# Optimization experiments

Measured on AMD Instinct MI355X. Metric: run time of the kernel, lower is better.

The kernel has to match this reference:

```python
import jax, jax.numpy as jnp
import numpy as np

B, N, H, W, NHOR = 4096, 128, 128, 64, 3

def setup_inputs() -> dict:
    key = jax.random.key(0)
    ks = jax.random.split(key, 11)
    s = 1.0 / np.sqrt(H)
    return {
        "embeddings": jax.random.normal(ks[0], (B, H), jnp.float32),
        "sensor_embeddings": jax.random.normal(ks[1], (B, N, H), jnp.float32),
        "sensor_logits": jax.random.normal(ks[2], (B, N), jnp.float32),
        "fc1_w": jax.random.normal(ks[3], (H, H), jnp.float32) * s,
        "fc1_b": jax.random.normal(ks[4], (H,), jnp.float32) * s,
        "fc2_w": jax.random.normal(ks[5], (NHOR * N, H), jnp.float32) * s,
        "fc2_b": jax.random.normal(ks[6], (NHOR * N,), jnp.float32) * s,
        "rw1": jax.random.normal(ks[7], (N, H, H), jnp.float32) * s,
        "rb1": jax.random.normal(ks[8], (N, H), jnp.float32) * s,
        "rw2": jax.random.normal(ks[9], (N, H, W), jnp.float32) * s,
        "rb2": jax.random.normal(ks[10], (N, W), jnp.float32) * s,
    }

def reference(embeddings, sensor_embeddings, sensor_logits,
              fc1_w, fc1_b, fc2_w, fc2_b, rw1, rb1, rw2, rb2):
    # Forecasting head: Linear -> ReLU -> (Dropout: identity in eval) -> Linear
    h = jax.nn.relu(embeddings @ fc1_w.T + fc1_b)              # (B, H)
    forecast = (h @ fc2_w.T + fc2_b).reshape(-1, NHOR, N)      # (B, NHOR, N)
    # Reconstruction heads: per-node MLPs batched as stacked GEMMs
    hn = jax.nn.relu(jnp.einsum('bnh,nhk->bnk', sensor_embeddings, rw1) + rb1)  # (B, N, H)
    recon = jnp.einsum('bnk,nkw->bnw', hn, rw2) + rb2          # (B, N, W)
    reconstruction = jnp.transpose(recon, (0, 2, 1))           # (B, W, N), matches torch.stack(dim=2)
    return (sensor_logits, forecast, reconstruction)
```

## Files before the change

### kernel.cpp

```cpp
#include <hip/hip_runtime.h>
#include <hip/hip_bf16.h>
#include <stdint.h>

typedef __attribute__((ext_vector_type(8))) short bf16x8;
typedef __attribute__((ext_vector_type(4))) float f32x4;

#define DEVI static __device__ __forceinline__

static constexpr int B_SZ = 4096, N_SZ = 128, H_SZ = 128, W_SZ = 64;

static constexpr size_t OFF_W1 = 0;
static constexpr size_t OFF_W2 = OFF_W1 + 4194304;
static constexpr size_t OFF_F1 = OFF_W2 + 2097152;
static constexpr size_t OFF_F2 = OFF_F1 + 32768;
static constexpr size_t OFF_H  = OFF_F2 + 98304;

DEVI unsigned short f2bf(float f) {
  union { __hip_bfloat16 b; unsigned short u; } cv;
  cv.b = __float2bfloat16(f);
  return cv.u;
}
DEVI float bf2f(unsigned short u) {
  union { unsigned int i; float f; } cv;
  cv.i = ((unsigned int)u) << 16;
  return cv.f;
}

DEVI void bar_lds() {
  __builtin_amdgcn_sched_barrier(0);
  asm volatile("s_waitcnt lgkmcnt(0)" ::: "memory");
  __builtin_amdgcn_s_barrier();
  __builtin_amdgcn_sched_barrier(0);
}

DEVI bf16x8 frag_ld(const unsigned char* base, int row, int kslot) {
  return *reinterpret_cast<const bf16x8*>(base + row * 256 + (((kslot ^ (row & 7)) << 4)));
}
DEVI bf16x8 gfrag_ld(const unsigned char* base, int row, int kslot) {
  return *reinterpret_cast<const bf16x8*>(base + row * 256 + (kslot << 4));
}

DEVI void stage_f32_tile(const float* src, int row_stride, unsigned char* dst, int tid, int nrows) {
  for (int t = tid; t < nrows * 16; t += 256) {
    int row = t >> 4, s = t & 15;
    const float* p = src + (size_t)row * row_stride + s * 8;
    union { unsigned short u[8]; uint4 v; } pk;
#pragma unroll
    for (int j = 0; j < 8; ++j) pk.u[j] = f2bf(p[j]);
    *reinterpret_cast<uint4*>(dst + row * 256 + ((s ^ (row & 7)) << 4)) = pk.v;
  }
}

__global__ __launch_bounds__(256) void prep_kernel(const float* __restrict__ rw1,
                                                   const float* __restrict__ rw2,
                                                   const float* __restrict__ fc1w,
                                                   const float* __restrict__ fc2w,
                                                   unsigned char* __restrict__ ws) {
  const int T_W1 = 128 * 128 * 16;
  const int T_W2 = 128 * 64 * 16;
  const int T_F1 = 128 * 16;
  const int T_F2 = 384 * 16;
  int id = blockIdx.x * 256 + threadIdx.x;
  if (id < T_W1) {
    int c = id & 127, rest = id >> 7;
    int s = rest & 15, n = rest >> 4;
    const float* src = rw1 + (size_t)n * 16384 + (size_t)(s * 8) * 128 + c;
    union { unsigned short u[8]; uint4 v; } pk;
#pragma unroll
    for (int j = 0; j < 8; ++j) pk.u[j] = f2bf(src[(size_t)j * 128]);
    size_t dst = OFF_W1 + ((size_t)n * 128 + c) * 256 + (size_t)(s << 4);
    *reinterpret_cast<uint4*>(ws + dst) = pk.v;
    return;
  }
  id -= T_W1;
  if (id < T_W2) {
    int w = id & 63, rest = id >> 6;
    int s = rest & 15, n = rest >> 4;
    const float* src = rw2 + (size_t)n * 8192 + (size_t)(s * 8) * 64 + w;
    union { unsigned short u[8]; uint4 v; } pk;
#pragma unroll
    for (int j = 0; j < 8; ++j) pk.u[j] = f2bf(src[(size_t)j * 64]);
    size_t dst = OFF_W2 + ((size_t)n * 64 + w) * 256 + (size_t)(s << 4);
    *reinterpret_cast<uint4*>(ws + dst) = pk.v;
    return;
  }
  id -= T_W2;
  if (id < T_F1) {
    int s = id & 15, o = id >> 4;
    const float* src = fc1w + (size_t)o * 128 + s * 8;
    union { unsigned short u[8]; uint4 v; } pk;
#pragma unroll
    for (int j = 0; j < 8; ++j) pk.u[j] = f2bf(src[j]);
    *reinterpret_cast<uint4*>(ws + OFF_F1 + (size_t)o * 256 + ((s ^ (o & 7)) << 4)) = pk.v;
    return;
  }
  id -= T_F1;
  if (id < T_F2) {
    int s = id & 15, o = id >> 4;
    const float* src = fc2w + (size_t)o * 128 + s * 8;
    union { unsigned short u[8]; uint4 v; } pk;
#pragma unroll
    for (int j = 0; j < 8; ++j) pk.u[j] = f2bf(src[j]);
    *reinterpret_cast<uint4*>(ws + OFF_F2 + (size_t)o * 256 + ((s ^ (o & 7)) << 4)) = pk.v;
  }
}

__global__ __launch_bounds__(256, 2) void recon_kernel(const float* __restrict__ se,
                                                       const float* __restrict__ rb1,
                                                       const float* __restrict__ rb2,
                                                       const unsigned char* __restrict__ ws,
                                                       float* __restrict__ out3) {
  __shared__ unsigned char sSE[2][16384];
  __shared__ unsigned char sHN[16384];

  const int tid = threadIdx.x;
  const int n = blockIdx.x;
  const int btg = blockIdx.y;
  const int b0 = btg * 512;

  const int wave = tid >> 6, lane = tid & 63;
  const int wm = wave >> 1, wq = wave & 1;
  const int lr = lane & 15, lk = lane >> 4;

  const unsigned char* w1b = ws + OFF_W1 + (size_t)n * 32768;
  const unsigned char* w2b = ws + OFF_W2 + (size_t)n * 16384;
  bf16x8 w1f[4][4], w2f[2][4];
#pragma unroll
  for (int m = 0; m < 4; ++m)
#pragma unroll
    for (int kk = 0; kk < 4; ++kk)
      w1f[m][kk] = gfrag_ld(w1b, wm * 64 + m * 16 + lr, kk * 4 + lk);
#pragma unroll
  for (int m = 0; m < 2; ++m)
#pragma unroll
    for (int kk = 0; kk < 4; ++kk)
      w2f[m][kk] = gfrag_ld(w2b, wm * 32 + m * 16 + lr, kk * 4 + lk);

  float bias1[4][4], bias2[2][4];
#pragma unroll
  for (int m = 0; m < 4; ++m)
#pragma unroll
    for (int j = 0; j < 4; ++j) bias1[m][j] = rb1[(size_t)n * 128 + wm * 64 + m * 16 + lk * 4 + j];
#pragma unroll
  for (int m = 0; m < 2; ++m)
#pragma unroll
    for (int j = 0; j < 4; ++j) bias2[m][j] = rb2[(size_t)n * 64 + wm * 32 + m * 16 + lk * 4 + j];

  stage_f32_tile(se + ((size_t)b0 * 128 + n) * 128, 128 * 128, sSE[0], tid, 64);
  unsigned short* outus = reinterpret_cast<unsigned short*>(out3);

  float4 fra[4], frb[4];
  {
    const float* sb = se + ((size_t)(b0 + 64) * 128 + n) * 128;
#pragma unroll
    for (int k = 0; k < 4; ++k) {
      int c = tid + k * 256;
      int row = c >> 4, s = c & 15;
      const float* p = sb + (size_t)row * 16384 + s * 8;
      fra[k] = *reinterpret_cast<const float4*>(p);
      frb[k] = *reinterpret_cast<const float4*>(p + 4);
    }
  }
  __syncthreads();

#pragma unroll 1
  for (int t = 0; t < 8; ++t) {
    unsigned char* bufc = sSE[t & 1];
    unsigned char* bufn = sSE[(t + 1) & 1];

    f32x4 acc[4][2] = {};
#pragma unroll
    for (int kk = 0; kk < 4; ++kk) {
      const int slot = kk * 4 + lk;
      bf16x8 bv[2];
#pragma unroll
      for (int q = 0; q < 2; ++q) bv[q] = frag_ld(bufc, wq * 32 + q * 16 + lr, slot);
#pragma unroll
      for (int m = 0; m < 4; ++m)
#pragma unroll
        for (int q = 0; q < 2; ++q)
          acc[m][q] = __builtin_amdgcn_mfma_f32_16x16x32_bf16(w1f[m][kk], bv[q], acc[m][q], 0, 0, 0);
    }
    bar_lds();

#pragma unroll
    for (int m = 0; m < 4; ++m) {
      const int k0 = wm * 64 + m * 16 + lk * 4;
      const int s16 = k0 >> 3, half = (k0 >> 2) & 1;
#pragma unroll
      for (int q = 0; q < 2; ++q) {
        const int b = wq * 32 + q * 16 + lr;
        union { unsigned short u[4]; uint2 v; } pk;
#pragma unroll
        for (int j = 0; j < 4; ++j) {
          float v = acc[m][q][j] + bias1[m][j];
          v = v > 0.f ? v : 0.f;
          pk.u[j] = f2bf(v);
        }
        *reinterpret_cast<uint2*>(sHN + b * 256 + ((s16 ^ (b & 7)) << 4) + half * 8) = pk.v;
      }
    }

    if (t < 7) {
#pragma unroll
      for (int k = 0; k < 4; ++k) {
        int c = tid + k * 256;
        int row = c >> 4, s = c & 15;
        union { unsigned short u[8]; uint4 v; } pk;
#pragma unroll
        for (int j = 0; j < 4; ++j) pk.u[j] = f2bf(fra[k][j]);
#pragma unroll
        for (int j = 0; j < 4; ++j) pk.u[4 + j] = f2bf(frb[k][j]);
        *reinterpret_cast<uint4*>(bufn + row * 256 + ((s ^ (row & 7)) << 4)) = pk.v;
      }
    }
    if (t < 6) {
      const float* sb = se + ((size_t)(b0 + (t + 2) * 64) * 128 + n) * 128;
#pragma unroll
      for (int k = 0; k < 4; ++k) {
        int c = tid + k * 256;
        int row = c >> 4, s = c & 15;
        const float* p = sb + (size_t)row * 16384 + s * 8;
        fra[k] = *reinterpret_cast<const float4*>(p);
        frb[k] = *reinterpret_cast<const float4*>(p + 4);
      }
    }
    bar_lds();

    f32x4 acc2[2][2] = {};
#pragma unroll
    for (int kk = 0; kk < 4; ++kk) {
      const int slot = kk * 4 + lk;
      bf16x8 bv[2];
#pragma unroll
      for (int q = 0; q < 2; ++q) bv[q] = frag_ld(sHN, wq * 32 + q * 16 + lr, slot);
#pragma unroll
      for (int m = 0; m < 2; ++m)
#pragma unroll
        for (int q = 0; q < 2; ++q)
          acc2[m][q] = __builtin_amdgcn_mfma_f32_16x16x32_bf16(w2f[m][kk], bv[q], acc2[m][q], 0, 0, 0);
    }

    const int bt0 = b0 + t * 64;
#pragma unroll
    for (int m = 0; m < 2; ++m) {
      const int w0 = wm * 32 + m * 16 + lk * 4;
#pragma unroll
      for (int q = 0; q < 2; ++q) {
        const int b = bt0 + wq * 32 + q * 16 + lr;
        union { unsigned short u[4]; uint2 v; } pk;
#pragma unroll
        for (int j = 0; j < 4; ++j) pk.u[j] = f2bf(acc2[m][q][j] + bias2[m][j]);
        *reinterpret_cast<uint2*>(outus + (size_t)b * 16384 + 8192 + n * 64 + w0) = pk.v;
      }
    }
  }
}

__global__ __launch_bounds__(256) void transpose_kernel(float* __restrict__ out3) {
  const int b = blockIdx.x, wave = threadIdx.x >> 6, lane = threadIdx.x & 63;
  const unsigned short* t = reinterpret_cast<const unsigned short*>(out3) + (size_t)b * 16384 + 8192;
  float* dst = out3 + (size_t)b * 8192;
  uint4 r[2][2];
#pragma unroll
  for (int half = 0; half < 2; ++half) {
    const int g = half * 4 + wave;
    r[half][0] = *reinterpret_cast<const uint4*>(t + lane * 64 + g * 8);
    r[half][1] = *reinterpret_cast<const uint4*>(t + (size_t)(lane + 64) * 64 + g * 8);
  }
  __syncthreads();
#pragma unroll
  for (int half = 0; half < 2; ++half) {
    const int g = half * 4 + wave;
    union { uint4 v; unsigned short u[8]; } p0, p1;
    p0.v = r[half][0];
    p1.v = r[half][1];
#pragma unroll
    for (int j = 0; j < 8; ++j) {
      dst[(g * 8 + j) * 128 + lane] = bf2f(p0.u[j]);
      dst[(g * 8 + j) * 128 + lane + 64] = bf2f(p1.u[j]);
    }
  }
}

__global__ __launch_bounds__(256) void f1_kernel(const float* __restrict__ emb,
                                                 const float* __restrict__ fc1b,
                                                 const unsigned char* __restrict__ ws,
                                                 unsigned char* __restrict__ hsw) {
  __shared__ unsigned char sA[32768];
  __shared__ unsigned char sB[32768];
  const int tid = threadIdx.x;
  const int bt = blockIdx.x;
  const int b0 = bt * 128;
  {
    const uint4* wp = reinterpret_cast<const uint4*>(ws + OFF_F1);
    uint4* d = reinterpret_cast<uint4*>(sB);
    for (int c = tid; c < 2048; c += 256) d[c] = wp[c];
  }
  stage_f32_tile(emb + (size_t)b0 * 128, 128, sA, tid, 128);
  __syncthreads();

  const int wave = tid >> 6, lane = tid & 63;
  const int wm = wave >> 1, wn = wave & 1;
  const int lr = lane & 15, lk = lane >> 4;

  f32x4 acc[4][4] = {};
#pragma unroll
  for (int kk = 0; kk < 4; ++kk) {
    bf16x8 af[4], bfv[4];
#pragma unroll
    for (int m = 0; m < 4; ++m) af[m] = frag_ld(sA, wm * 64 + m * 16 + lr, kk * 4 + lk);
#pragma unroll
    for (int q = 0; q < 4; ++q) bfv[q] = frag_ld(sB, wn * 64 + q * 16 + lr, kk * 4 + lk);
#pragma unroll
    for (int m = 0; m < 4; ++m)
#pragma unroll
      for (int q = 0; q < 4; ++q)
        acc[m][q] = __builtin_amdgcn_mfma_f32_16x16x32_bf16(af[m], bfv[q], acc[m][q], 0, 0, 0);
  }

  unsigned char* tile = hsw + (size_t)bt * 32768;
#pragma unroll
  for (int q = 0; q < 4; ++q) {
    int c = wn * 64 + q * 16 + lr;
    float bias = fc1b[c];
#pragma unroll
    for (int m = 0; m < 4; ++m) {
#pragma unroll
      for (int j = 0; j < 4; ++j) {
        int r = wm * 64 + m * 16 + lk * 4 + j;
        float v = acc[m][q][j] + bias;
        v = v > 0.f ? v : 0.f;
        *reinterpret_cast<unsigned short*>(tile + r * 256 + ((c * 2) ^ ((r & 7) << 4))) = f2bf(v);
      }
    }
  }
}

__global__ __launch_bounds__(256) void f2_kernel(const unsigned char* __restrict__ hsw,
                                                 const unsigned char* __restrict__ f2s,
                                                 const float* __restrict__ fc2b,
                                                 float* __restrict__ out2) {
  __shared__ unsigned char sA[32768];
  __shared__ unsigned char sB[32768];
  const int tid = threadIdx.x;
  const int bt = blockIdx.x;
  const int ch = blockIdx.y;
  const int b0 = bt * 128;
  {
    const uint4* ap = reinterpret_cast<const uint4*>(hsw + (size_t)bt * 32768);
    uint4* da = reinterpret_cast<uint4*>(sA);
    for (int c = tid; c < 2048; c += 256) da[c] = ap[c];
    const uint4* bp = reinterpret_cast<const uint4*>(f2s + (size_t)ch * 32768);
    uint4* db = reinterpret_cast<uint4*>(sB);
    for (int c = tid; c < 2048; c += 256) db[c] = bp[c];
  }
  __syncthreads();

  const int wave = tid >> 6, lane = tid & 63;
  const int wm = wave >> 1, wn = wave & 1;
  const int lr = lane & 15, lk = lane >> 4;

  f32x4 acc[4][4] = {};
#pragma unroll
  for (int kk = 0; kk < 4; ++kk) {
    bf16x8 af[4], bfv[4];
#pragma unroll
    for (int m = 0; m < 4; ++m) af[m] = frag_ld(sA, wm * 64 + m * 16 + lr, kk * 4 + lk);
#pragma unroll
    for (int q = 0; q < 4; ++q) bfv[q] = frag_ld(sB, wn * 64 + q * 16 + lr, kk * 4 + lk);
#pragma unroll
    for (int m = 0; m < 4; ++m)
#pragma unroll
      for (int q = 0; q < 4; ++q)
        acc[m][q] = __builtin_amdgcn_mfma_f32_16x16x32_bf16(af[m], bfv[q], acc[m][q], 0, 0, 0);
  }

#pragma unroll
  for (int q = 0; q < 4; ++q) {
    int o = ch * 128 + wn * 64 + q * 16 + lr;
    float bias = fc2b[o];
#pragma unroll
    for (int m = 0; m < 4; ++m) {
#pragma unroll
      for (int j = 0; j < 4; ++j) {
        int r = wm * 64 + m * 16 + lk * 4 + j;
        out2[(size_t)(b0 + r) * 384 + o] = acc[m][q][j] + bias;
      }
    }
  }
}

extern "C" void kernel_launch(void* const* d_in, const int* in_sizes, int n_in,
                              void* d_out, int out_size, void* d_ws, size_t ws_size,
                              hipStream_t stream) {
  const float* emb  = (const float*)d_in[0];
  const float* se   = (const float*)d_in[1];
  const float* slog = (const float*)d_in[2];
  const float* fc1w = (const float*)d_in[3];
  const float* fc1b = (const float*)d_in[4];
  const float* fc2w = (const float*)d_in[5];
  const float* fc2b = (const float*)d_in[6];
  const float* rw1  = (const float*)d_in[7];
  const float* rb1  = (const float*)d_in[8];
  const float* rw2  = (const float*)d_in[9];
  const float* rb2  = (const float*)d_in[10];
  float* out = (float*)d_out;
  unsigned char* ws = (unsigned char*)d_ws;

  hipMemcpyAsync(out, slog, (size_t)B_SZ * N_SZ * sizeof(float),
                 hipMemcpyDeviceToDevice, stream);

  prep_kernel<<<1568, 256, 0, stream>>>(rw1, rw2, fc1w, fc2w, ws);

  f1_kernel<<<32, 256, 0, stream>>>(emb, fc1b, ws, ws + OFF_H);
  f2_kernel<<<dim3(32, 3), 256, 0, stream>>>(ws + OFF_H, ws + OFF_F2, fc2b,
                                             out + (size_t)B_SZ * N_SZ);

  float* out3 = out + (size_t)B_SZ * N_SZ + (size_t)B_SZ * 384;
  recon_kernel<<<dim3(128, 8), 256, 0, stream>>>(se, rb1, rb2, ws, out3);
  transpose_kernel<<<4096, 256, 0, stream>>>(out3);
}
```

Measured before the change: 138.9 us.

## Stage sensor embeddings via async global-to-LDS loads and fold logits copy into prep

Replaces the register-staged fp32 loads, conversion and LDS stores of the sensor-embedding tiles with async global_load_lds transfers that write raw fp32 into a larger, swizzled double buffer. Conversion to bf16 now happens at fragment-load time, and explicit vmcnt waits pace the pipeline. This aims to free registers and VALU from the staging path and overlap loads better. It also replaces the separate memcpy of sensor_logits with extra threads in prep_kernel to save a launch. The cost is doubled LDS use (64KB for the two buffers plus sHN), which may lower occupancy, and more conversion work inside the MFMA loop.

```diff
diff --git a/kernel.cpp b/kernel.cpp
--- a/kernel.cpp
+++ b/kernel.cpp
@@ -15,6 +15,9 @@
 static constexpr size_t OFF_F2 = OFF_F1 + 32768;
 static constexpr size_t OFF_H  = OFF_F2 + 98304;
 
+typedef const __attribute__((address_space(1))) void gvoid;
+typedef __attribute__((address_space(3))) void lvoid;
+
 DEVI unsigned short f2bf(float f) {
   union { __hip_bfloat16 b; unsigned short u; } cv;
   cv.b = __float2bfloat16(f);
@@ -51,15 +54,32 @@
   }
 }
 
+DEVI void stage_async(const float* se, int brow0, int n, unsigned char* dstbase,
+                      int wave, int lane) {
+  const int rr = lane >> 5;
+  const int g  = lane & 31;
+#pragma unroll
+  for (int c = 0; c < 8; ++c) {
+    const int rl = wave * 16 + c * 2 + rr;
+    const int gsrc = g ^ ((rl & 7) << 1);
+    const float* gp = se + ((size_t)(brow0 + rl) * 128 + n) * 128 + gsrc * 4;
+    unsigned char* lp = dstbase + (wave * 16 + c * 2) * 512;
+    __builtin_amdgcn_global_load_lds((gvoid*)gp, (lvoid*)lp, 16, 0, 0);
+  }
+}
+
 __global__ __launch_bounds__(256) void prep_kernel(const float* __restrict__ rw1,
                                                    const float* __restrict__ rw2,
                                                    const float* __restrict__ fc1w,
                                                    const float* __restrict__ fc2w,
+                                                   const float* __restrict__ slog,
+                                                   float* __restrict__ out,
                                                    unsigned char* __restrict__ ws) {
   const int T_W1 = 128 * 128 * 16;
   const int T_W2 = 128 * 64 * 16;
   const int T_F1 = 128 * 16;
   const int T_F2 = 384 * 16;
+  const int T_LG = 131072;
   int id = blockIdx.x * 256 + threadIdx.x;
   if (id < T_W1) {
     int c = id & 127, rest = id >> 7;
@@ -102,6 +122,11 @@
 #pragma unroll
     for (int j = 0; j < 8; ++j) pk.u[j] = f2bf(src[j]);
     *reinterpret_cast<uint4*>(ws + OFF_F2 + (size_t)o * 256 + ((s ^ (o & 7)) << 4)) = pk.v;
+    return;
+  }
+  id -= T_F2;
+  if (id < T_LG) {
+    reinterpret_cast<uint4*>(out)[id] = reinterpret_cast<const uint4*>(slog)[id];
   }
 }
 
@@ -110,7 +135,7 @@
                                                        const float* __restrict__ rb2,
                                                        const unsigned char* __restrict__ ws,
                                                        float* __restrict__ out3) {
-  __shared__ unsigned char sSE[2][16384];
+  __shared__ unsigned char sSE[2][32768];
   __shared__ unsigned char sHN[16384];
 
   const int tid = threadIdx.x;
@@ -146,27 +171,21 @@
 #pragma unroll
     for (int j = 0; j < 4; ++j) bias2[m][j] = rb2[(size_t)n * 64 + wm * 32 + m * 16 + lk * 4 + j];
 
-  stage_f32_tile(se + ((size_t)b0 * 128 + n) * 128, 128 * 128, sSE[0], tid, 64);
   unsigned short* outus = reinterpret_cast<unsigned short*>(out3);
 
-  float4 fra[4], frb[4];
-  {
-    const float* sb = se + ((size_t)(b0 + 64) * 128 + n) * 128;
-#pragma unroll
-    for (int k = 0; k < 4; ++k) {
-      int c = tid + k * 256;
-      int row = c >> 4, s = c & 15;
-      const float* p = sb + (size_t)row * 16384 + s * 8;
-      fra[k] = *reinterpret_cast<const float4*>(p);
-      frb[k] = *reinterpret_cast<const float4*>(p + 4);
-    }
-  }
-  __syncthreads();
+  stage_async(se, b0, n, sSE[0], wave, lane);
+  stage_async(se, b0 + 64, n, sSE[1], wave, lane);
 
 #pragma unroll 1
   for (int t = 0; t < 8; ++t) {
     unsigned char* bufc = sSE[t & 1];
-    unsigned char* bufn = sSE[(t + 1) & 1];
+
+    __builtin_amdgcn_sched_barrier(0);
+    if (t == 0 || t == 7) asm volatile("s_waitcnt vmcnt(8)" ::: "memory");
+    else if (t == 1)      asm volatile("s_waitcnt vmcnt(12)" ::: "memory");
+    else                  asm volatile("s_waitcnt vmcnt(16)" ::: "memory");
+    __builtin_amdgcn_s_barrier();
+    __builtin_amdgcn_sched_barrier(0);
 
     f32x4 acc[4][2] = {};
 #pragma unroll
@@ -174,7 +193,16 @@
       const int slot = kk * 4 + lk;
       bf16x8 bv[2];
 #pragma unroll
-      for (int q = 0; q < 2; ++q) bv[q] = frag_ld(bufc, wq * 32 + q * 16 + lr, slot);
+      for (int q = 0; q < 2; ++q) {
+        const int b = wq * 32 + q * 16 + lr;
+        const unsigned char* base = bufc + b * 512 + (((2 * slot) ^ ((b & 7) << 1)) << 4);
+        float4 lo = *reinterpret_cast<const float4*>(base);
+        float4 hi = *reinterpret_cast<const float4*>(base + 16);
+        union { unsigned short u[8]; bf16x8 v; } pk;
+        pk.u[0] = f2bf(lo.x); pk.u[1] = f2bf(lo.y); pk.u[2] = f2bf(lo.z); pk.u[3] = f2bf(lo.w);
+        pk.u[4] = f2bf(hi.x); pk.u[5] = f2bf(hi.y); pk.u[6] = f2bf(hi.z); pk.u[7] = f2bf(hi.w);
+        bv[q] = pk.v;
+      }
 #pragma unroll
       for (int m = 0; m < 4; ++m)
 #pragma unroll
@@ -182,6 +210,8 @@
           acc[m][q] = __builtin_amdgcn_mfma_f32_16x16x32_bf16(w1f[m][kk], bv[q], acc[m][q], 0, 0, 0);
     }
     bar_lds();
+
+    if (t < 6) stage_async(se, b0 + (t + 2) * 64, n, bufc, wave, lane);
 
 #pragma unroll
     for (int m = 0; m < 4; ++m) {
@@ -198,31 +228,6 @@
           pk.u[j] = f2bf(v);
         }
         *reinterpret_cast<uint2*>(sHN + b * 256 + ((s16 ^ (b & 7)) << 4) + half * 8) = pk.v;
-      }
-    }
-
-    if (t < 7) {
-#pragma unroll
-      for (int k = 0; k < 4; ++k) {
-        int c = tid + k * 256;
-        int row = c >> 4, s = c & 15;
-        union { unsigned short u[8]; uint4 v; } pk;
-#pragma unroll
-        for (int j = 0; j < 4; ++j) pk.u[j] = f2bf(fra[k][j]);
-#pragma unroll
-        for (int j = 0; j < 4; ++j) pk.u[4 + j] = f2bf(frb[k][j]);
-        *reinterpret_cast<uint4*>(bufn + row * 256 + ((s ^ (row & 7)) << 4)) = pk.v;
-      }
-    }
-    if (t < 6) {
-      const float* sb = se + ((size_t)(b0 + (t + 2) * 64) * 128 + n) * 128;
-#pragma unroll
-      for (int k = 0; k < 4; ++k) {
-        int c = tid + k * 256;
-        int row = c >> 4, s = c & 15;
-        const float* p = sb + (size_t)row * 16384 + s * 8;
-        fra[k] = *reinterpret_cast<const float4*>(p);
-        frb[k] = *reinterpret_cast<const float4*>(p + 4);
       }
     }
     bar_lds();
@@ -408,10 +413,7 @@
   float* out = (float*)d_out;
   unsigned char* ws = (unsigned char*)d_ws;
 
-  hipMemcpyAsync(out, slog, (size_t)B_SZ * N_SZ * sizeof(float),
-                 hipMemcpyDeviceToDevice, stream);
-
-  prep_kernel<<<1568, 256, 0, stream>>>(rw1, rw2, fc1w, fc2w, ws);
+  prep_kernel<<<2080, 256, 0, stream>>>(rw1, rw2, fc1w, fc2w, slog, out, ws);
 
   f1_kernel<<<32, 256, 0, stream>>>(emb, fc1b, ws, ws + OFF_H);
   f2_kernel<<<dim3(32, 3), 256, 0, stream>>>(ws + OFF_H, ws + OFF_F2, fc2b,
```

Result: slower. 147.7 us (+6.4%).

## Merge prep, f1, memcpy into one launch and co-schedule f2 with recon

Applied to the files above, without the earlier changes.

Cuts the launch count from five kernels plus a memcpy down to three. The weight-prep kernel now also copies the sensor logits and runs the fc1 GEMM in extra blocks that convert fc1 weights on the fly. The f2 GEMM runs as extra blocks of the recon kernel and reads its A operand directly from global memory rather than from LDS. Recon now takes its biases from shared memory and reloads its W2 fragments every iteration to lower register pressure, at the cost of more repeated global or L2 reads.

```diff
diff --git a/kernel.cpp b/kernel.cpp
--- a/kernel.cpp
+++ b/kernel.cpp
@@ -51,102 +51,192 @@
   }
 }
 
-__global__ __launch_bounds__(256) void prep_kernel(const float* __restrict__ rw1,
-                                                   const float* __restrict__ rw2,
-                                                   const float* __restrict__ fc1w,
-                                                   const float* __restrict__ fc2w,
-                                                   unsigned char* __restrict__ ws) {
-  const int T_W1 = 128 * 128 * 16;
-  const int T_W2 = 128 * 64 * 16;
-  const int T_F1 = 128 * 16;
-  const int T_F2 = 384 * 16;
-  int id = blockIdx.x * 256 + threadIdx.x;
-  if (id < T_W1) {
-    int c = id & 127, rest = id >> 7;
-    int s = rest & 15, n = rest >> 4;
-    const float* src = rw1 + (size_t)n * 16384 + (size_t)(s * 8) * 128 + c;
-    union { unsigned short u[8]; uint4 v; } pk;
-#pragma unroll
-    for (int j = 0; j < 8; ++j) pk.u[j] = f2bf(src[(size_t)j * 128]);
-    size_t dst = OFF_W1 + ((size_t)n * 128 + c) * 256 + (size_t)(s << 4);
-    *reinterpret_cast<uint4*>(ws + dst) = pk.v;
+__global__ __launch_bounds__(256) void prep_f1_kernel(const float* __restrict__ rw1,
+                                                      const float* __restrict__ rw2,
+                                                      const float* __restrict__ fc2w,
+                                                      const float* __restrict__ slog,
+                                                      const float* __restrict__ emb,
+                                                      const float* __restrict__ fc1w,
+                                                      const float* __restrict__ fc1b,
+                                                      float* __restrict__ out,
+                                                      unsigned char* __restrict__ ws) {
+  __shared__ unsigned char sA[16384];
+  __shared__ unsigned char sB[32768];
+
+  const int bid = blockIdx.x;
+  const int tid = threadIdx.x;
+  if (bid < 2072) {
+    const int T_W1 = 128 * 128 * 16;
+    const int T_W2 = 128 * 64 * 16;
+    const int T_F2 = 384 * 16;
+    int id = bid * 256 + tid;
+    if (id < T_W1) {
+      int c = id & 127, rest = id >> 7;
+      int s = rest & 15, n = rest >> 4;
+      const float* src = rw1 + (size_t)n * 16384 + (size_t)(s * 8) * 128 + c;
+      union { unsigned short u[8]; uint4 v; } pk;
+#pragma unroll
+      for (int j = 0; j < 8; ++j) pk.u[j] = f2bf(src[(size_t)j * 128]);
+      size_t dst = OFF_W1 + ((size_t)n * 128 + c) * 256 + (size_t)(s << 4);
+      *reinterpret_cast<uint4*>(ws + dst) = pk.v;
+      return;
+    }
+    id -= T_W1;
+    if (id < T_W2) {
+      int w = id & 63, rest = id >> 6;
+      int s = rest & 15, n = rest >> 4;
+      const float* src = rw2 + (size_t)n * 8192 + (size_t)(s * 8) * 64 + w;
+      union { unsigned short u[8]; uint4 v; } pk;
+#pragma unroll
+      for (int j = 0; j < 8; ++j) pk.u[j] = f2bf(src[(size_t)j * 64]);
+      size_t dst = OFF_W2 + ((size_t)n * 64 + w) * 256 + (size_t)(s << 4);
+      *reinterpret_cast<uint4*>(ws + dst) = pk.v;
+      return;
+    }
+    id -= T_W2;
+    if (id < T_F2) {
+      int s = id & 15, o = id >> 4;
+      const float* src = fc2w + (size_t)o * 128 + s * 8;
+      union { unsigned short u[8]; uint4 v; } pk;
+#pragma unroll
+      for (int j = 0; j < 8; ++j) pk.u[j] = f2bf(src[j]);
+      *reinterpret_cast<uint4*>(ws + OFF_F2 + (size_t)o * 256 + ((s ^ (o & 7)) << 4)) = pk.v;
+      return;
+    }
+    id -= T_F2;
+    reinterpret_cast<uint4*>(out)[id] = reinterpret_cast<const uint4*>(slog)[id];
     return;
   }
-  id -= T_W1;
-  if (id < T_W2) {
-    int w = id & 63, rest = id >> 6;
-    int s = rest & 15, n = rest >> 4;
-    const float* src = rw2 + (size_t)n * 8192 + (size_t)(s * 8) * 64 + w;
-    union { unsigned short u[8]; uint4 v; } pk;
-#pragma unroll
-    for (int j = 0; j < 8; ++j) pk.u[j] = f2bf(src[(size_t)j * 64]);
-    size_t dst = OFF_W2 + ((size_t)n * 64 + w) * 256 + (size_t)(s << 4);
-    *reinterpret_cast<uint4*>(ws + dst) = pk.v;
+
+  const int bt = bid - 2072;
+  const int b0 = bt * 64;
+  stage_f32_tile(fc1w, 128, sB, tid, 128);
+  stage_f32_tile(emb + (size_t)b0 * 128, 128, sA, tid, 64);
+  __syncthreads();
+
+  const int wave = tid >> 6, lane = tid & 63;
+  const int wm = wave >> 1, wn = wave & 1;
+  const int lr = lane & 15, lk = lane >> 4;
+
+  f32x4 acc[2][4] = {};
+#pragma unroll
+  for (int kk = 0; kk < 4; ++kk) {
+    const int slot = kk * 4 + lk;
+    bf16x8 af[2], bfv[4];
+#pragma unroll
+    for (int m = 0; m < 2; ++m) af[m] = frag_ld(sA, wm * 32 + m * 16 + lr, slot);
+#pragma unroll
+    for (int q = 0; q < 4; ++q) bfv[q] = frag_ld(sB, wn * 64 + q * 16 + lr, slot);
+#pragma unroll
+    for (int m = 0; m < 2; ++m)
+#pragma unroll
+      for (int q = 0; q < 4; ++q)
+        acc[m][q] = __builtin_amdgcn_mfma_f32_16x16x32_bf16(af[m], bfv[q], acc[m][q], 0, 0, 0);
+  }
+
+  unsigned char* tile = ws + OFF_H + (size_t)bt * 16384;
+#pragma unroll
+  for (int q = 0; q < 4; ++q) {
+    int c = wn * 64 + q * 16 + lr;
+    float bias = fc1b[c];
+#pragma unroll
+    for (int m = 0; m < 2; ++m) {
+#pragma unroll
+      for (int j = 0; j < 4; ++j) {
+        int r = wm * 32 + m * 16 + lk * 4 + j;
+        float v = acc[m][q][j] + bias;
+        v = v > 0.f ? v : 0.f;
+        *reinterpret_cast<unsigned short*>(tile + r * 256 + ((c * 2) ^ ((r & 7) << 4))) = f2bf(v);
+      }
+    }
+  }
+}
+
+__global__ __launch_bounds__(256, 2) void recon_f2_kernel(const float* __restrict__ se,
+                                                          const float* __restrict__ rb1,
+                                                          const float* __restrict__ rb2,
+                                                          const float* __restrict__ fc2b,
+                                                          const unsigned char* __restrict__ ws,
+                                                          float* __restrict__ out3,
+                                                          float* __restrict__ out2) {
+  __shared__ unsigned char smem[49920];
+
+  const int bid = blockIdx.x;
+  const int tid = threadIdx.x;
+  const int wave = tid >> 6, lane = tid & 63;
+  const int lr = lane & 15, lk = lane >> 4;
+
+  if (bid >= 1024) {
+    const int fid = bid - 1024;
+    const int bt = fid & 63, ch = fid >> 6;
+    const int b0 = bt * 64;
+    unsigned char* sB = smem;
+    {
+      const uint4* bp = reinterpret_cast<const uint4*>(ws + OFF_F2 + (size_t)ch * 32768);
+      uint4* db = reinterpret_cast<uint4*>(sB);
+      for (int c = tid; c < 2048; c += 256) db[c] = bp[c];
+    }
+    __syncthreads();
+
+    const int wm = wave >> 1, wn = wave & 1;
+    const unsigned char* htile = ws + OFF_H + (size_t)bt * 16384;
+
+    f32x4 acc[2][4] = {};
+#pragma unroll
+    for (int kk = 0; kk < 4; ++kk) {
+      const int slot = kk * 4 + lk;
+      bf16x8 af[2], bfv[4];
+#pragma unroll
+      for (int m = 0; m < 2; ++m) af[m] = frag_ld(htile, wm * 32 + m * 16 + lr, slot);
+#pragma unroll
+      for (int q = 0; q < 4; ++q) bfv[q] = frag_ld(sB, wn * 64 + q * 16 + lr, slot);
+#pragma unroll
+      for (int m = 0; m < 2; ++m)
+#pragma unroll
+        for (int q = 0; q < 4; ++q)
+          acc[m][q] = __builtin_amdgcn_mfma_f32_16x16x32_bf16(af[m], bfv[q], acc[m][q], 0, 0, 0);
+    }
+
+#pragma unroll
+    for (int q = 0; q < 4; ++q) {
+      int o = ch * 128 + wn * 64 + q * 16 + lr;
+      float bias = fc2b[o];
+#pragma unroll
+      for (int m = 0; m < 2; ++m) {
+#pragma unroll
+        for (int j = 0; j < 4; ++j) {
+          int r = wm * 32 + m * 16 + lk * 4 + j;
+          out2[(size_t)(b0 + r) * 384 + o] = acc[m][q][j] + bias;
+        }
+      }
+    }
     return;
   }
-  id -= T_W2;
-  if (id < T_F1) {
-    int s = id & 15, o = id >> 4;
-    const float* src = fc1w + (size_t)o * 128 + s * 8;
-    union { unsigned short u[8]; uint4 v; } pk;
-#pragma unroll
-    for (int j = 0; j < 8; ++j) pk.u[j] = f2bf(src[j]);
-    *reinterpret_cast<uint4*>(ws + OFF_F1 + (size_t)o * 256 + ((s ^ (o & 7)) << 4)) = pk.v;
-    return;
-  }
-  id -= T_F1;
-  if (id < T_F2) {
-    int s = id & 15, o = id >> 4;
-    const float* src = fc2w + (size_t)o * 128 + s * 8;
-    union { unsigned short u[8]; uint4 v; } pk;
-#pragma unroll
-    for (int j = 0; j < 8; ++j) pk.u[j] = f2bf(src[j]);
-    *reinterpret_cast<uint4*>(ws + OFF_F2 + (size_t)o * 256 + ((s ^ (o & 7)) << 4)) = pk.v;
-  }
-}
-
-__global__ __launch_bounds__(256, 2) void recon_kernel(const float* __restrict__ se,
-                                                       const float* __restrict__ rb1,
-                                                       const float* __restrict__ rb2,
-                                                       const unsigned char* __restrict__ ws,
-                                                       float* __restrict__ out3) {
-  __shared__ unsigned char sSE[2][16384];
-  __shared__ unsigned char sHN[16384];
-
-  const int tid = threadIdx.x;
-  const int n = blockIdx.x;
-  const int btg = blockIdx.y;
+
+  unsigned char* sSE0 = smem;
+  unsigned char* sSE1 = smem + 16384;
+  unsigned char* sHN = smem + 32768;
+  float* sBIAS = reinterpret_cast<float*>(smem + 49152);
+
+  const int n = bid & 127;
+  const int btg = bid >> 7;
   const int b0 = btg * 512;
 
-  const int wave = tid >> 6, lane = tid & 63;
   const int wm = wave >> 1, wq = wave & 1;
-  const int lr = lane & 15, lk = lane >> 4;
 
   const unsigned char* w1b = ws + OFF_W1 + (size_t)n * 32768;
   const unsigned char* w2b = ws + OFF_W2 + (size_t)n * 16384;
-  bf16x8 w1f[4][4], w2f[2][4];
+  bf16x8 w1f[4][4];
 #pragma unroll
   for (int m = 0; m < 4; ++m)
 #pragma unroll
     for (int kk = 0; kk < 4; ++kk)
       w1f[m][kk] = gfrag_ld(w1b, wm * 64 + m * 16 + lr, kk * 4 + lk);
-#pragma unroll
-  for (int m = 0; m < 2; ++m)
-#pragma unroll
-    for (int kk = 0; kk < 4; ++kk)
-      w2f[m][kk] = gfrag_ld(w2b, wm * 32 + m * 16 + lr, kk * 4 + lk);
-
-  float bias1[4][4], bias2[2][4];
-#pragma unroll
-  for (int m = 0; m < 4; ++m)
-#pragma unroll
-    for (int j = 0; j < 4; ++j) bias1[m][j] = rb1[(size_t)n * 128 + wm * 64 + m * 16 + lk * 4 + j];
-#pragma unroll
-  for (int m = 0; m < 2; ++m)
-#pragma unroll
-    for (int j = 0; j < 4; ++j) bias2[m][j] = rb2[(size_t)n * 64 + wm * 32 + m * 16 + lk * 4 + j];
-
-  stage_f32_tile(se + ((size_t)b0 * 128 + n) * 128, 128 * 128, sSE[0], tid, 64);
+
+  if (tid < 192)
+    sBIAS[tid] = (tid < 128) ? rb1[(size_t)n * 128 + tid] : rb2[(size_t)n * 64 + tid - 128];
+
+  stage_f32_tile(se + ((size_t)b0 * 128 + n) * 128, 128 * 128, sSE0, tid, 64);
   unsigned short* outus = reinterpret_cast<unsigned short*>(out3);
 
   float4 fra[4], frb[4];
@@ -161,12 +251,12 @@
       frb[k] = *reinterpret_cast<const float4*>(p + 4);
     }
   }
-  __syncthreads();
+  bar_lds();
 
 #pragma unroll 1
   for (int t = 0; t < 8; ++t) {
-    unsigned char* bufc = sSE[t & 1];
-    unsigned char* bufn = sSE[(t + 1) & 1];
+    unsigned char* bufc = (t & 1) ? sSE1 : sSE0;
+    unsigned char* bufn = (t & 1) ? sSE0 : sSE1;
 
     f32x4 acc[4][2] = {};
 #pragma unroll
@@ -182,24 +272,6 @@
           acc[m][q] = __builtin_amdgcn_mfma_f32_16x16x32_bf16(w1f[m][kk], bv[q], acc[m][q], 0, 0, 0);
     }
     bar_lds();
-
-#pragma unroll
-    for (int m = 0; m < 4; ++m) {
-      const int k0 = wm * 64 + m * 16 + lk * 4;
-      const int s16 = k0 >> 3, half = (k0 >> 2) & 1;
-#pragma unroll
-      for (int q = 0; q < 2; ++q) {
-        const int b = wq * 32 + q * 16 + lr;
-        union { unsigned short u[4]; uint2 v; } pk;
-#pragma unroll
-        for (int j = 0; j < 4; ++j) {
-          float v = acc[m][q][j] + bias1[m][j];
-          v = v > 0.f ? v : 0.f;
-          pk.u[j] = f2bf(v);
-        }
-        *reinterpret_cast<uint2*>(sHN + b * 256 + ((s16 ^ (b & 7)) << 4) + half * 8) = pk.v;
-      }
-    }
 
     if (t < 7) {
 #pragma unroll
@@ -225,6 +297,32 @@
         frb[k] = *reinterpret_cast<const float4*>(p + 4);
       }
     }
+    bf16x8 w2f[2][4];
+#pragma unroll
+    for (int m = 0; m < 2; ++m)
+#pragma unroll
+      for (int kk = 0; kk < 4; ++kk)
+        w2f[m][kk] = gfrag_ld(w2b, wm * 32 + m * 16 + lr, kk * 4 + lk);
+
+#pragma unroll
+    for (int m = 0; m < 4; ++m) {
+      const int k0 = wm * 64 + m * 16 + lk * 4;
+      const int s16 = k0 >> 3, half = (k0 >> 2) & 1;
+      union { float4 v; float f[4]; } b1;
+      b1.v = *reinterpret_cast<const float4*>(sBIAS + k0);
+#pragma unroll
+      for (int q = 0; q < 2; ++q) {
+        const int b = wq * 32 + q * 16 + lr;
+        union { unsigned short u[4]; uint2 v; } pk;
+#pragma unroll
+        for (int j = 0; j < 4; ++j) {
+          float v = acc[m][q][j] + b1.f[j];
+          v = v > 0.f ? v : 0.f;
+          pk.u[j] = f2bf(v);
+        }
+        *reinterpret_cast<uint2*>(sHN + b * 256 + ((s16 ^ (b & 7)) << 4) + half * 8) = pk.v;
+      }
+    }
     bar_lds();
 
     f32x4 acc2[2][2] = {};
@@ -245,12 +343,14 @@
 #pragma unroll
     for (int m = 0; m < 2; ++m) {
       const int w0 = wm * 32 + m * 16 + lk * 4;
+      union { float4 v; float f[4]; } b2;
+      b2.v = *reinterpret_cast<const float4*>(sBIAS + 128 + w0);
 #pragma unroll
       for (int q = 0; q < 2; ++q) {
         const int b = bt0 + wq * 32 + q * 16 + lr;
         union { unsigned short u[4]; uint2 v; } pk;
 #pragma unroll
-        for (int j = 0; j < 4; ++j) pk.u[j] = f2bf(acc2[m][q][j] + bias2[m][j]);
+        for (int j = 0; j < 4; ++j) pk.u[j] = f2bf(acc2[m][q][j] + b2.f[j]);
         *reinterpret_cast<uint2*>(outus + (size_t)b * 16384 + 8192 + n * 64 + w0) = pk.v;
       }
     }
@@ -279,114 +379,6 @@
     for (int j = 0; j < 8; ++j) {
       dst[(g * 8 + j) * 128 + lane] = bf2f(p0.u[j]);
       dst[(g * 8 + j) * 128 + lane + 64] = bf2f(p1.u[j]);
-    }
-  }
-}
-
-__global__ __launch_bounds__(256) void f1_kernel(const float* __restrict__ emb,
-                                                 const float* __restrict__ fc1b,
-                                                 const unsigned char* __restrict__ ws,
-                                                 unsigned char* __restrict__ hsw) {
-  __shared__ unsigned char sA[32768];
-  __shared__ unsigned char sB[32768];
-  const int tid = threadIdx.x;
-  const int bt = blockIdx.x;
-  const int b0 = bt * 128;
-  {
-    const uint4* wp = reinterpret_cast<const uint4*>(ws + OFF_F1);
-    uint4* d = reinterpret_cast<uint4*>(sB);
-    for (int c = tid; c < 2048; c += 256) d[c] = wp[c];
-  }
-  stage_f32_tile(emb + (size_t)b0 * 128, 128, sA, tid, 128);
-  __syncthreads();
-
-  const int wave = tid >> 6, lane = tid & 63;
-  const int wm = wave >> 1, wn = wave & 1;
-  const int lr = lane & 15, lk = lane >> 4;
-
-  f32x4 acc[4][4] = {};
-#pragma unroll
-  for (int kk = 0; kk < 4; ++kk) {
-    bf16x8 af[4], bfv[4];
-#pragma unroll
-    for (int m = 0; m < 4; ++m) af[m] = frag_ld(sA, wm * 64 + m * 16 + lr, kk * 4 + lk);
-#pragma unroll
-    for (int q = 0; q < 4; ++q) bfv[q] = frag_ld(sB, wn * 64 + q * 16 + lr, kk * 4 + lk);
-#pragma unroll
-    for (int m = 0; m < 4; ++m)
-#pragma unroll
-      for (int q = 0; q < 4; ++q)
-        acc[m][q] = __builtin_amdgcn_mfma_f32_16x16x32_bf16(af[m], bfv[q], acc[m][q], 0, 0, 0);
-  }
-
-  unsigned char* tile = hsw + (size_t)bt * 32768;
-#pragma unroll
-  for (int q = 0; q < 4; ++q) {
-    int c = wn * 64 + q * 16 + lr;
-    float bias = fc1b[c];
-#pragma unroll
-    for (int m = 0; m < 4; ++m) {
-#pragma unroll
-      for (int j = 0; j < 4; ++j) {
-        int r = wm * 64 + m * 16 + lk * 4 + j;
-        float v = acc[m][q][j] + bias;
-        v = v > 0.f ? v : 0.f;
-        *reinterpret_cast<unsigned short*>(tile + r * 256 + ((c * 2) ^ ((r & 7) << 4))) = f2bf(v);
-      }
-    }
-  }
-}
-
-__global__ __launch_bounds__(256) void f2_kernel(const unsigned char* __restrict__ hsw,
-                                                 const unsigned char* __restrict__ f2s,
-                                                 const float* __restrict__ fc2b,
-                                                 float* __restrict__ out2) {
-  __shared__ unsigned char sA[32768];
-  __shared__ unsigned char sB[32768];
-  const int tid = threadIdx.x;
-  const int bt = blockIdx.x;
-  const int ch = blockIdx.y;
-  const int b0 = bt * 128;
-  {
-    const uint4* ap = reinterpret_cast<const uint4*>(hsw + (size_t)bt * 32768);
-    uint4* da = reinterpret_cast<uint4*>(sA);
-    for (int c = tid; c < 2048; c += 256) da[c] = ap[c];
-    const uint4* bp = reinterpret_cast<const uint4*>(f2s + (size_t)ch * 32768);
-    uint4* db = reinterpret_cast<uint4*>(sB);
-    for (int c = tid; c < 2048; c += 256) db[c] = bp[c];
-  }
-  __syncthreads();
-
-  const int wave = tid >> 6, lane = tid & 63;
-  const int wm = wave >> 1, wn = wave & 1;
-  const int lr = lane & 15, lk = lane >> 4;
-
-  f32x4 acc[4][4] = {};
-#pragma unroll
-  for (int kk = 0; kk < 4; ++kk) {
-    bf16x8 af[4], bfv[4];
-#pragma unroll
-    for (int m = 0; m < 4; ++m) af[m] = frag_ld(sA, wm * 64 + m * 16 + lr, kk * 4 + lk);
-#pragma unroll
-    for (int q = 0; q < 4; ++q) bfv[q] = frag_ld(sB, wn * 64 + q * 16 + lr, kk * 4 + lk);
-#pragma unroll
-    for (int m = 0; m < 4; ++m)
-#pragma unroll
-      for (int q = 0; q < 4; ++q)
-        acc[m][q] = __builtin_amdgcn_mfma_f32_16x16x32_bf16(af[m], bfv[q], acc[m][q], 0, 0, 0);
-  }
-
-#pragma unroll
-  for (int q = 0; q < 4; ++q) {
-    int o = ch * 128 + wn * 64 + q * 16 + lr;
-    float bias = fc2b[o];
-#pragma unroll
-    for (int m = 0; m < 4; ++m) {
-#pragma unroll
-      for (int j = 0; j < 4; ++j) {
-        int r = wm * 64 + m * 16 + lk * 4 + j;
-        out2[(size_t)(b0 + r) * 384 + o] = acc[m][q][j] + bias;
-      }
     }
   }
 }
@@ -408,16 +400,12 @@
   float* out = (float*)d_out;
   unsigned char* ws = (unsigned char*)d_ws;
 
-  hipMemcpyAsync(out, slog, (size_t)B_SZ * N_SZ * sizeof(float),
-                 hipMemcpyDeviceToDevice, stream);
-
-  prep_kernel<<<1568, 256, 0, stream>>>(rw1, rw2, fc1w, fc2w, ws);
-
-  f1_kernel<<<32, 256, 0, stream>>>(emb, fc1b, ws, ws + OFF_H);
-  f2_kernel<<<dim3(32, 3), 256, 0, stream>>>(ws + OFF_H, ws + OFF_F2, fc2b,
-                                             out + (size_t)B_SZ * N_SZ);
-
-  float* out3 = out + (size_t)B_SZ * N_SZ + (size_t)B_SZ * 384;
-  recon_kernel<<<dim3(128, 8), 256, 0, stream>>>(se, rb1, rb2, ws, out3);
+  float* out2 = out + (size_t)B_SZ * N_SZ;
+  float* out3 = out2 + (size_t)B_SZ * 384;
+
+  prep_f1_kernel<<<2136, 256, 0, stream>>>(rw1, rw2, fc2w, slog, emb, fc1w, fc1b, out, ws);
+
+  recon_f2_kernel<<<1216, 256, 0, stream>>>(se, rb1, rb2, fc2b, ws, out3, out2);
+
   transpose_kernel<<<4096, 256, 0, stream>>>(out3);
 }
```

Result: no change. 136.2 us (-1.9%).
